# Optimization experiments

Hardware: AMD Instinct MI355X
Metric: run time of the kernel (lower is better)

The kernel has to match this reference:

```python
import jax, jax.numpy as jnp
import numpy as np

SIZE = 100
NUM_PARAMS = 5
DEPTH = 10            # complete binary tree: 2**DEPTH - 1 = 1023 nodes, 512 leaves
NUM_TREES = 1024
NUM_NODES = 2 ** DEPTH - 1


def setup_inputs() -> dict:
    key = jax.random.key(0)
    ks = jax.random.split(key, 7)
    times = jax.random.uniform(ks[0], (NUM_TREES, NUM_NODES), dtype=jnp.float32) + 0.1
    # Linear(1, size): weight column vector + bias
    Qw = jax.random.normal(ks[1], (SIZE,), dtype=jnp.float32) * 0.5
    Qb = jax.random.normal(ks[2], (SIZE,), dtype=jnp.float32) * 0.1
    # Linear(size, size): scaled so deep relu chain stays stable
    Ww = jax.random.normal(ks[3], (SIZE, SIZE), dtype=jnp.float32) * (0.5 / np.sqrt(SIZE))
    Wb = jax.random.normal(ks[4], (SIZE,), dtype=jnp.float32) * 0.1
    # Linear(size, num_params)
    Pw = jax.random.normal(ks[5], (NUM_PARAMS, SIZE), dtype=jnp.float32) * (1.0 / np.sqrt(SIZE))
    Pb = jax.random.normal(ks[6], (NUM_PARAMS,), dtype=jnp.float32) * 0.1
    return {"times": times, "Qw": Qw, "Qb": Qb, "Ww": Ww, "Wb": Wb, "Pw": Pw, "Pb": Pb}


def reference(times, Qw, Qb, Ww, Wb, Pw, Pb):
    """Batched, level-synchronous version of gRNN.traverse over complete binary trees.

    times: [B, 2**D - 1] node times in heap order (node i -> children 2i+1, 2i+2).
    Leaf:     h = relu(Q(t))
    Internal: h = relu(W(h_left + h_right) + Q(t))
    Root output projected to num_params. Same math as the recursive torch code.
    """
    B, N = times.shape
    D = int(np.log2(N + 1))
    # leaf level (deepest): Q(t) = t * Qw + Qb  (Linear(1, size))
    s = 2 ** (D - 1) - 1
    h = jax.nn.relu(times[:, s:s + 2 ** (D - 1), None] * Qw + Qb)  # [B, 2^(D-1), size]
    for d in range(D - 2, -1, -1):  # fixed small loop over tree depth
        s = 2 ** d - 1
        t = times[:, s:s + 2 ** d, None]                 # [B, 2^d, 1]
        comb = h[:, 0::2] + h[:, 1::2]                   # left + right children
        h = jax.nn.relu(jnp.einsum('bns,os->bno', comb, Ww) + Wb + t * Qw + Qb)
    root = h[:, 0]                                       # [B, size]
    return root @ Pw.T + Pb                              # [B, num_params]
```

## Files before the change

### kernel.cpp

```cpp
#include <hip/hip_runtime.h>

typedef _Float16 h8 __attribute__((ext_vector_type(8)));
typedef _Float16 h4 __attribute__((ext_vector_type(4)));
typedef _Float16 h2 __attribute__((ext_vector_type(2)));
typedef float f4 __attribute__((ext_vector_type(4)));
typedef float f16v __attribute__((ext_vector_type(16)));

#define HSTRIDE 104

__global__ __launch_bounds__(64, 1)
void grnn_fused(const float* __restrict__ times,
                const float* __restrict__ Qw,
                const float* __restrict__ Qb,
                const float* __restrict__ Ww,
                const float* __restrict__ Wb,
                const float* __restrict__ Pw,
                const float* __restrict__ Pb,
                float* __restrict__ out)
{
  __shared__ __align__(16) _Float16 Cs[128][HSTRIDE];
  __shared__ __align__(16) _Float16 trash[512];
  __shared__ __align__(4)  _Float16 ts_fold[512];
  __shared__ __align__(4)  h2 tsp[256];
  __shared__ __align__(16) _Float16 qwh[112];
  __shared__ __align__(16) _Float16 qbh[112];

  const int lane = threadIdx.x;
  const int c    = lane & 31;
  const int hw   = lane >> 5;
  const int tree = blockIdx.x;

  {
    const float* tg = times + tree * 1023;
    #pragma unroll
    for (int q = 0; q < 8; ++q) {
      const int ix = lane + 64 * q;
      if (ix < 511) ts_fold[ix] = (_Float16)tg[ix];
    }
    #pragma unroll
    for (int q = 0; q < 4; ++q) {
      const int pr = lane + 64 * q;
      tsp[pr] = (h2){(_Float16)tg[511 + 2 * pr], (_Float16)tg[512 + 2 * pr]};
    }
    #pragma unroll
    for (int q = 0; q < 2; ++q) {
      const int ix = lane + 64 * q;
      if (ix < 112) {
        qwh[ix] = (ix < 100) ? (_Float16)Qw[ix] : (_Float16)0.f;
        qbh[ix] = (ix < 100) ? (_Float16)Qb[ix] : (_Float16)0.f;
      }
    }
  }

  h8 wf[4][7];
  #pragma unroll
  for (int ft = 0; ft < 4; ++ft) {
    const int r = 32 * ft + c;
    #pragma unroll
    for (int kc = 0; kc < 7; ++kc) {
      h8 v;
      #pragma unroll
      for (int j = 0; j < 8; ++j) v[j] = (_Float16)0.f;
      if (r < 100) {
        if (kc < 6) {
          const int kb = 16 * kc + 8 * hw;
          const f4 w0 = *(const f4*)&Ww[r * 100 + kb];
          const f4 w1 = *(const f4*)&Ww[r * 100 + kb + 4];
          #pragma unroll
          for (int j = 0; j < 4; ++j) {
            v[j]     = (_Float16)w0[j];
            v[j + 4] = (_Float16)w1[j];
          }
        } else if (hw == 0) {
          const f4 w0 = *(const f4*)&Ww[r * 100 + 96];
          #pragma unroll
          for (int j = 0; j < 4; ++j) v[j] = (_Float16)w0[j];
          v[4] = (_Float16)Qw[r];
          v[5] = (_Float16)(Qb[r] + Wb[r]);
        }
      }
      wf[ft][kc] = v;
    }
  }

#define DO_TILE(BF, BSE, DODPP) do {                                          \
    f16v acc_[4];                                                             \
    _Pragma("unroll")                                                         \
    for (int ft_ = 0; ft_ < 4; ++ft_)                                         \
      _Pragma("unroll")                                                       \
      for (int e_ = 0; e_ < 16; ++e_) acc_[ft_][e_] = 0.f;                    \
    _Pragma("unroll")                                                         \
    for (int kc_ = 0; kc_ < 7; ++kc_) {                                       \
      _Pragma("unroll")                                                       \
      for (int ft_ = 0; ft_ < 4; ++ft_)                                       \
        acc_[ft_] = __builtin_amdgcn_mfma_f32_32x32x16_f16(wf[ft_][kc_],      \
                                              BF[kc_], acc_[ft_], 0, 0, 0);   \
    }                                                                         \
    _Float16* b3_ = (hw == 0) ? (BSE) : &trash[lane * 4];                     \
    _Pragma("unroll")                                                         \
    for (int ft_ = 0; ft_ < 4; ++ft_) {                                       \
      _Pragma("unroll")                                                       \
      for (int g_ = 0; g_ < 4; ++g_) {                                        \
        if (ft_ < 3 || (g_ == 0)) {                                           \
          float a0_ = fmaxf(acc_[ft_][4 * g_ + 0], 0.f);                      \
          float a1_ = fmaxf(acc_[ft_][4 * g_ + 1], 0.f);                      \
          float a2_ = fmaxf(acc_[ft_][4 * g_ + 2], 0.f);                      \
          float a3_ = fmaxf(acc_[ft_][4 * g_ + 3], 0.f);                      \
          h2 lo_ = __builtin_bit_cast(h2,                                     \
                       __builtin_amdgcn_cvt_pkrtz(a0_, a1_));                 \
          h2 hi_ = __builtin_bit_cast(h2,                                     \
                       __builtin_amdgcn_cvt_pkrtz(a2_, a3_));                 \
          if (DODPP) {                                                        \
            int d0_ = __builtin_amdgcn_mov_dpp(__builtin_bit_cast(int, lo_),  \
                                               0xB1, 0xF, 0xF, true);         \
            int d1_ = __builtin_amdgcn_mov_dpp(__builtin_bit_cast(int, hi_),  \
                                               0xB1, 0xF, 0xF, true);         \
            lo_ = lo_ + __builtin_bit_cast(h2, d0_);                          \
            hi_ = hi_ + __builtin_bit_cast(h2, d1_);                          \
          }                                                                   \
          h4 hv_ = {lo_[0], lo_[1], hi_[0], hi_[1]};                          \
          *(h4*)(((ft_ == 3) ? b3_ : (BSE)) + 32 * ft_ + 8 * g_ + 4 * hw)     \
              = hv_;                                                          \
        }                                                                     \
      }                                                                       \
    }                                                                         \
  } while (0)

#define LOAD_B(BF, RBASE, RMASK, TSIB) do {                                   \
    const int cm_ = c & (RMASK);                                              \
    const int row_ = (RBASE) + cm_;                                           \
    _Pragma("unroll")                                                         \
    for (int kc_ = 0; kc_ < 6; ++kc_)                                         \
      BF[kc_] = *(const h8*)&Cs[row_][16 * kc_ + 8 * hw];                     \
    if (hw == 0) {                                                            \
      h4 lo_ = *(const h4*)&Cs[row_][96];                                     \
      h4 hi_ = {ts_fold[(TSIB) + cm_], (_Float16)1.f,                         \
                (_Float16)0.f, (_Float16)0.f};                                \
      BF[6] = __builtin_shufflevector(lo_, hi_, 0, 1, 2, 3, 4, 5, 6, 7);      \
    } else {                                                                  \
      _Pragma("unroll")                                                       \
      for (int j_ = 0; j_ < 8; ++j_) BF[6][j_] = (_Float16)0.f;               \
    }                                                                         \
  } while (0)

#define BASE_PTR(WROW, NN)                                                    \
    ((((c & 1) == 0) && (c < (NN))) ? &Cs[(WROW) + (c >> 1)][0]               \
                                    : &trash[lane * 4])

  #pragma unroll 2
  for (int i = 0; i < 8; ++i) {
    const h2 tp = tsp[32 * i + c];
    const _Float16 t0 = tp[0], t1 = tp[1];
    const h8 z8 = {(_Float16)0.f, (_Float16)0.f, (_Float16)0.f, (_Float16)0.f,
                   (_Float16)0.f, (_Float16)0.f, (_Float16)0.f, (_Float16)0.f};
    h8 bf[7];
    #pragma unroll
    for (int kc = 0; kc < 7; ++kc) {
      const h8 qw8 = *(const h8*)&qwh[16 * kc + 8 * hw];
      const h8 qb8 = *(const h8*)&qbh[16 * kc + 8 * hw];
      h8 a = __builtin_elementwise_max(qw8 * t0 + qb8, z8);
      h8 b = __builtin_elementwise_max(qw8 * t1 + qb8, z8);
      bf[kc] = a + b;
    }
    if (hw == 0) {
      bf[6][4] = ts_fold[255 + 32 * i + c];
      bf[6][5] = (_Float16)1.f;
    }
    _Float16* bse = BASE_PTR(16 * i, 32);
    DO_TILE(bf, bse, 1);
  }

  #pragma unroll 1
  for (int i = 0; i < 4; ++i) {
    h8 bf[7];
    LOAD_B(bf, 32 * i, 31, 127 + 32 * i);
    _Float16* bse = BASE_PTR(16 * i, 32);
    DO_TILE(bf, bse, 1);
  }
  #pragma unroll 1
  for (int i = 0; i < 2; ++i) {
    h8 bf[7];
    LOAD_B(bf, 32 * i, 31, 63 + 32 * i);
    _Float16* bse = BASE_PTR(16 * i, 32);
    DO_TILE(bf, bse, 1);
  }
  {
    h8 bf[7];
    LOAD_B(bf, 0, 31, 31);
    _Float16* bse = BASE_PTR(0, 32);
    DO_TILE(bf, bse, 1);
  }
  #pragma unroll 1
  for (int d = 4; d >= 1; --d) {
    const int nn = 1 << d;
    h8 bf[7];
    LOAD_B(bf, 0, nn - 1, nn - 1);
    _Float16* bse = BASE_PTR(0, nn);
    DO_TILE(bf, bse, 1);
  }
  {
    h8 bf[7];
    LOAD_B(bf, 0, 0, 0);
    _Float16* bse = (c == 0) ? &Cs[0][0] : &trash[lane * 4];
    DO_TILE(bf, bse, 0);
  }

  #pragma unroll 1
  for (int p = 0; p < 5; ++p) {
    float v = (float)Cs[0][lane] * Pw[p * 100 + lane];
    if (lane < 36) v += (float)Cs[0][64 + lane] * Pw[p * 100 + 64 + lane];
    v += __shfl_xor(v, 32, 64);
    v += __shfl_xor(v, 16, 64);
    v += __shfl_xor(v, 8, 64);
    v += __shfl_xor(v, 4, 64);
    v += __shfl_xor(v, 2, 64);
    v += __shfl_xor(v, 1, 64);
    if (lane == 0) out[tree * 5 + p] = v + Pb[p];
  }
#undef DO_TILE
#undef LOAD_B
#undef BASE_PTR
}

extern "C" void kernel_launch(void* const* d_in, const int* in_sizes, int n_in,
                              void* d_out, int out_size, void* d_ws, size_t ws_size,
                              hipStream_t stream) {
  (void)n_in; (void)out_size; (void)d_ws; (void)ws_size;
  const float* times = (const float*)d_in[0];
  const float* Qw = (const float*)d_in[1];
  const float* Qb = (const float*)d_in[2];
  const float* Ww = (const float*)d_in[3];
  const float* Wb = (const float*)d_in[4];
  const float* Pw = (const float*)d_in[5];
  const float* Pb = (const float*)d_in[6];
  float* outp = (float*)d_out;
  const int B = in_sizes[0] / 1023;
  grnn_fused<<<dim3(B), dim3(64), 0, stream>>>(times, Qw, Qb, Ww, Wb, Pw, Pb, outp);
}
```

Baseline: 98.17 us.

## Double-buffer B fragments across tiles and keep Q params in registers

Fully unrolls the leaf level and the next three internal levels into a two-buffer schedule. The next tile's B operands (leaf ReLU build or LDS loads) are issued before the current tile's MFMAs, so LDS latency and VALU work can overlap with matrix-core work. Qw/Qb are also converted once into per-lane h8 registers instead of being staged in LDS and reloaded for every leaf tile. This raises register pressure and code size, which could cause spills or hurt scheduling.

```diff
diff --git a/kernel.cpp b/kernel.cpp
--- a/kernel.cpp
+++ b/kernel.cpp
@@ -22,8 +22,6 @@
   __shared__ __align__(16) _Float16 trash[512];
   __shared__ __align__(4)  _Float16 ts_fold[512];
   __shared__ __align__(4)  h2 tsp[256];
-  __shared__ __align__(16) _Float16 qwh[112];
-  __shared__ __align__(16) _Float16 qbh[112];
 
   const int lane = threadIdx.x;
   const int c    = lane & 31;
@@ -41,14 +39,6 @@
     for (int q = 0; q < 4; ++q) {
       const int pr = lane + 64 * q;
       tsp[pr] = (h2){(_Float16)tg[511 + 2 * pr], (_Float16)tg[512 + 2 * pr]};
-    }
-    #pragma unroll
-    for (int q = 0; q < 2; ++q) {
-      const int ix = lane + 64 * q;
-      if (ix < 112) {
-        qwh[ix] = (ix < 100) ? (_Float16)Qw[ix] : (_Float16)0.f;
-        qbh[ix] = (ix < 100) ? (_Float16)Qb[ix] : (_Float16)0.f;
-      }
     }
   }
 
@@ -83,6 +73,17 @@
     }
   }
 
+  h8 qwp[7], qbp[7];
+  #pragma unroll
+  for (int kc = 0; kc < 7; ++kc) {
+    #pragma unroll
+    for (int j = 0; j < 8; ++j) {
+      const int ix = 16 * kc + 8 * hw + j;
+      qwp[kc][j] = (ix < 100) ? (_Float16)Qw[ix] : (_Float16)0.f;
+      qbp[kc][j] = (ix < 100) ? (_Float16)Qb[ix] : (_Float16)0.f;
+    }
+  }
+
 #define DO_TILE(BF, BSE, DODPP) do {                                          \
     f16v acc_[4];                                                             \
     _Pragma("unroll")                                                         \
@@ -143,66 +144,66 @@
     }                                                                         \
   } while (0)
 
+#define LEAF_BUILD(BF, I) do {                                                \
+    const h2 tp_ = tsp[32 * (I) + c];                                         \
+    const _Float16 t0_ = tp_[0], t1_ = tp_[1];                                \
+    const h8 z8_ = {(_Float16)0.f, (_Float16)0.f, (_Float16)0.f,              \
+                    (_Float16)0.f, (_Float16)0.f, (_Float16)0.f,              \
+                    (_Float16)0.f, (_Float16)0.f};                            \
+    _Pragma("unroll")                                                         \
+    for (int kc_ = 0; kc_ < 7; ++kc_) {                                       \
+      h8 a_ = __builtin_elementwise_max(qwp[kc_] * t0_ + qbp[kc_], z8_);      \
+      h8 b_ = __builtin_elementwise_max(qwp[kc_] * t1_ + qbp[kc_], z8_);      \
+      BF[kc_] = a_ + b_;                                                      \
+    }                                                                         \
+    if (hw == 0) {                                                            \
+      BF[6][4] = ts_fold[255 + 32 * (I) + c];                                 \
+      BF[6][5] = (_Float16)1.f;                                               \
+    }                                                                         \
+  } while (0)
+
 #define BASE_PTR(WROW, NN)                                                    \
     ((((c & 1) == 0) && (c < (NN))) ? &Cs[(WROW) + (c >> 1)][0]               \
                                     : &trash[lane * 4])
 
-  #pragma unroll 2
-  for (int i = 0; i < 8; ++i) {
-    const h2 tp = tsp[32 * i + c];
-    const _Float16 t0 = tp[0], t1 = tp[1];
-    const h8 z8 = {(_Float16)0.f, (_Float16)0.f, (_Float16)0.f, (_Float16)0.f,
-                   (_Float16)0.f, (_Float16)0.f, (_Float16)0.f, (_Float16)0.f};
-    h8 bf[7];
-    #pragma unroll
-    for (int kc = 0; kc < 7; ++kc) {
-      const h8 qw8 = *(const h8*)&qwh[16 * kc + 8 * hw];
-      const h8 qb8 = *(const h8*)&qbh[16 * kc + 8 * hw];
-      h8 a = __builtin_elementwise_max(qw8 * t0 + qb8, z8);
-      h8 b = __builtin_elementwise_max(qw8 * t1 + qb8, z8);
-      bf[kc] = a + b;
-    }
-    if (hw == 0) {
-      bf[6][4] = ts_fold[255 + 32 * i + c];
-      bf[6][5] = (_Float16)1.f;
-    }
-    _Float16* bse = BASE_PTR(16 * i, 32);
-    DO_TILE(bf, bse, 1);
-  }
-
-  #pragma unroll 1
-  for (int i = 0; i < 4; ++i) {
-    h8 bf[7];
-    LOAD_B(bf, 32 * i, 31, 127 + 32 * i);
-    _Float16* bse = BASE_PTR(16 * i, 32);
-    DO_TILE(bf, bse, 1);
-  }
-  #pragma unroll 1
-  for (int i = 0; i < 2; ++i) {
-    h8 bf[7];
-    LOAD_B(bf, 32 * i, 31, 63 + 32 * i);
-    _Float16* bse = BASE_PTR(16 * i, 32);
-    DO_TILE(bf, bse, 1);
-  }
-  {
-    h8 bf[7];
-    LOAD_B(bf, 0, 31, 31);
-    _Float16* bse = BASE_PTR(0, 32);
-    DO_TILE(bf, bse, 1);
-  }
+  h8 bfA[7], bfB[7];
+
+  LEAF_BUILD(bfA, 0);
+  LEAF_BUILD(bfB, 1);  DO_TILE(bfA, BASE_PTR(0, 32), 1);
+  LEAF_BUILD(bfA, 2);  DO_TILE(bfB, BASE_PTR(16, 32), 1);
+  LEAF_BUILD(bfB, 3);  DO_TILE(bfA, BASE_PTR(32, 32), 1);
+  LEAF_BUILD(bfA, 4);  DO_TILE(bfB, BASE_PTR(48, 32), 1);
+  LEAF_BUILD(bfB, 5);  DO_TILE(bfA, BASE_PTR(64, 32), 1);
+  LEAF_BUILD(bfA, 6);  DO_TILE(bfB, BASE_PTR(80, 32), 1);
+  LEAF_BUILD(bfB, 7);  DO_TILE(bfA, BASE_PTR(96, 32), 1);
+                       DO_TILE(bfB, BASE_PTR(112, 32), 1);
+
+  LOAD_B(bfA, 0, 31, 127);
+  LOAD_B(bfB, 32, 31, 159);
+  DO_TILE(bfA, BASE_PTR(0, 32), 1);
+  LOAD_B(bfA, 64, 31, 191);
+  DO_TILE(bfB, BASE_PTR(16, 32), 1);
+  LOAD_B(bfB, 96, 31, 223);
+  DO_TILE(bfA, BASE_PTR(32, 32), 1);
+  LOAD_B(bfA, 0, 31, 63);
+  DO_TILE(bfB, BASE_PTR(48, 32), 1);
+  LOAD_B(bfB, 32, 31, 95);
+  DO_TILE(bfA, BASE_PTR(0, 32), 1);
+  DO_TILE(bfB, BASE_PTR(16, 32), 1);
+  LOAD_B(bfA, 0, 31, 31);
+  DO_TILE(bfA, BASE_PTR(0, 32), 1);
+
   #pragma unroll 1
   for (int d = 4; d >= 1; --d) {
     const int nn = 1 << d;
-    h8 bf[7];
-    LOAD_B(bf, 0, nn - 1, nn - 1);
+    LOAD_B(bfA, 0, nn - 1, nn - 1);
     _Float16* bse = BASE_PTR(0, nn);
-    DO_TILE(bf, bse, 1);
+    DO_TILE(bfA, bse, 1);
   }
   {
-    h8 bf[7];
-    LOAD_B(bf, 0, 0, 0);
+    LOAD_B(bfA, 0, 0, 0);
     _Float16* bse = (c == 0) ? &Cs[0][0] : &trash[lane * 4];
-    DO_TILE(bf, bse, 0);
+    DO_TILE(bfA, bse, 0);
   }
 
   #pragma unroll 1
@@ -219,6 +220,7 @@
   }
 #undef DO_TILE
 #undef LOAD_B
+#undef LEAF_BUILD
 #undef BASE_PTR
 }
 
```

New measurement: 100.8 us. 2.7% more time.
